# Performance work log

Hardware: AMD Instinct MI355X
Metric: run time of the kernel (lower is better)

## Reference

```python
import jax, jax.numpy as jnp
import numpy as np

N = 50000   # nodes
E = 800000  # edges
H = 128     # hidden_dim
H2 = H // 2


def setup_inputs() -> dict:
    key = jax.random.key(0)
    ks = jax.random.split(key, 12)
    s = 0.05  # weight scale for numerical sanity
    d = {}
    d['coord_x'] = jax.random.normal(ks[0], (N,), jnp.float32)
    d['coord_y'] = jax.random.normal(ks[1], (N,), jnp.float32)
    d['W1'] = jax.random.normal(ks[2], (3, H), jnp.float32) * s
    d['b1'] = jnp.zeros((H,), jnp.float32)
    d['W2'] = jax.random.normal(ks[3], (H, H), jnp.float32) * s
    d['b2'] = jnp.zeros((H,), jnp.float32)
    d['W3'] = jax.random.normal(ks[4], (H, H), jnp.float32) * s
    d['b3'] = jnp.zeros((H,), jnp.float32)
    d['W4'] = jax.random.normal(ks[5], (H, H), jnp.float32) * s
    d['b4'] = jnp.zeros((H,), jnp.float32)
    d['W5'] = jax.random.normal(ks[6], (H, H), jnp.float32) * s
    d['b5'] = jnp.zeros((H,), jnp.float32)
    d['Wl1'] = jax.random.normal(ks[7], (H, H2), jnp.float32) * s
    d['bl1'] = jnp.zeros((H2,), jnp.float32)
    d['Wl2'] = jax.random.normal(ks[8], (H2, 1), jnp.float32) * s
    d['bl2'] = jnp.zeros((1,), jnp.float32)
    d['src'] = jax.random.randint(ks[9], (E,), 0, N, dtype=jnp.int32)
    d['dst'] = jax.random.randint(ks[10], (E,), 0, N, dtype=jnp.int32)
    return d


def reference(coord_x, coord_y, W1, b1, W2, b2, W3, b3, W4, b4, W5, b5,
              Wl1, bl1, Wl2, bl2, src, dst):
    ones_e = jnp.ones((E,), jnp.float32)
    in_deg = jax.ops.segment_sum(ones_e, dst, num_segments=N)   # [N]
    out_deg = jax.ops.segment_sum(ones_e, src, num_segments=N)  # [N]
    # DGL GraphConv norm='both': D_out^{-1/2} on src side, D_in^{-1/2} on dst side,
    # degrees clamped to min 1.
    norm_s = (jnp.maximum(out_deg, 1.0) ** -0.5)[:, None]  # [N,1]
    norm_d = (jnp.maximum(in_deg, 1.0) ** -0.5)[:, None]   # [N,1]

    def gconv(h, W, b):
        msg = (h * norm_s)[src]                                   # [E,F] gather
        agg = jax.ops.segment_sum(msg, dst, num_segments=N)       # [N,F] scatter-add
        return (agg * norm_d) @ W + b

    # node features: [in_degree, x, y]
    h = jnp.stack([in_deg, coord_x, coord_y], axis=1)  # [N,3]
    for W, b in ((W1, b1), (W2, b2), (W3, b3), (W4, b4), (W5, b5)):
        h = jax.nn.relu(gconv(h, W, b))

    graph_emb = jnp.mean(h, axis=0, keepdims=True)          # [1,H] mean_nodes
    h_emb = jax.nn.relu(graph_emb @ Wl1 + bl1)              # dropout p=0 -> identity
    pred = jax.nn.sigmoid(h_emb @ Wl2 + bl2)                # [1,1]
    return pred, graph_emb, h
```

## Files before the change

### kernel.cpp

```cpp
#include <hip/hip_runtime.h>
#include <hip/hip_bf16.h>
#include <math.h>

#define NN 50000
#define NE 800000
#define HD 128
#define NB 196
#define CAP 5120
#define B1_EPB 1024

typedef __attribute__((ext_vector_type(8))) short bf16x8v;
typedef __attribute__((ext_vector_type(4))) float f32x4v;

static __device__ __forceinline__ unsigned short f2bf(float x) {
    union { float f; unsigned u; } v; v.f = x;
    unsigned r = v.u + 0x7fff + ((v.u >> 16) & 1);
    return (unsigned short)(r >> 16);
}

__global__ __launch_bounds__(256) void bucket_kernel(const int* __restrict__ src,
                                                     const int* __restrict__ dst,
                                                     int* __restrict__ dcur,
                                                     int* __restrict__ scur,
                                                     ushort2* __restrict__ dbucket,
                                                     unsigned short* __restrict__ sbucket) {
    __shared__ int hd[NB], hsb[NB], cd[NB], cs[NB];
    int t = threadIdx.x;
    if (t < NB) { hd[t] = 0; hsb[t] = 0; }
    __syncthreads();
    int d[4], s[4];
    int e0 = blockIdx.x * B1_EPB + t;
    #pragma unroll
    for (int j = 0; j < 4; ++j) {
        int e = e0 + j * 256;
        if (e < NE) {
            d[j] = dst[e]; s[j] = src[e];
            atomicAdd(&hd[d[j] >> 8], 1);
            atomicAdd(&hsb[s[j] >> 8], 1);
        } else d[j] = -1;
    }
    __syncthreads();
    if (t < NB) {
        cd[t] = atomicAdd(&dcur[t], hd[t]);
        cs[t] = atomicAdd(&scur[t], hsb[t]);
    }
    __syncthreads();
    #pragma unroll
    for (int j = 0; j < 4; ++j) {
        if (d[j] >= 0) {
            int b = d[j] >> 8;
            int p = atomicAdd(&cd[b], 1);
            if (p < CAP) dbucket[(long)b * CAP + p] = make_ushort2((unsigned short)d[j],
                                                                   (unsigned short)s[j]);
            int bs = s[j] >> 8;
            int p2 = atomicAdd(&cs[bs], 1);
            if (p2 < CAP) sbucket[(long)bs * CAP + p2] = (unsigned short)s[j];
        }
    }
}

__global__ __launch_bounds__(256) void csr_out_kernel(const ushort2* __restrict__ dbucket,
                                                      const int* __restrict__ dcur,
                                                      const unsigned short* __restrict__ sbucket,
                                                      const int* __restrict__ scur,
                                                      int* __restrict__ row_ptr,
                                                      unsigned short* __restrict__ col,
                                                      int* __restrict__ out_cnt) {
    __shared__ int buf[256];
    __shared__ int hist[256];
    __shared__ int cur[256];
    int k = blockIdx.x, t = threadIdx.x;

    int tot = (t < NB) ? min(dcur[t], CAP) : 0;
    buf[t] = tot;
    __syncthreads();
    for (int o = 1; o < 256; o <<= 1) {
        int a = (t >= o) ? buf[t - o] : 0;
        __syncthreads();
        buf[t] += a;
        __syncthreads();
    }
    int base = (k > 0) ? buf[k - 1] : 0;
    int cnt = min(dcur[k], CAP);

    hist[t] = 0;
    __syncthreads();
    const ushort2* bk = dbucket + (long)k * CAP;
    for (int e = t; e < cnt; e += 256) atomicAdd(&hist[bk[e].x & 255], 1);
    __syncthreads();
    int h = hist[t];

    buf[t] = h;
    __syncthreads();
    for (int o = 1; o < 256; o <<= 1) {
        int a = (t >= o) ? buf[t - o] : 0;
        __syncthreads();
        buf[t] += a;
        __syncthreads();
    }
    int start = base + buf[t] - h;
    int id = (k << 8) + t;
    if (id < NN) row_ptr[id] = start;
    if (k == NB - 1 && t == 0) row_ptr[NN] = base + cnt;
    cur[t] = start;
    __syncthreads();

    for (int e = t; e < cnt; e += 256) {
        ushort2 p = bk[e];
        int pos = atomicAdd(&cur[p.x & 255], 1);
        col[pos] = p.y;
    }

    __syncthreads();
    hist[t] = 0;
    __syncthreads();
    int scnt = min(scur[k], CAP);
    const unsigned short* sk = sbucket + (long)k * CAP;
    for (int e = t; e < scnt; e += 256) atomicAdd(&hist[sk[e] & 255], 1);
    __syncthreads();
    if (id < NN) out_cnt[id] = hist[t];
}

__global__ __launch_bounds__(256) void initw_kernel(const float* __restrict__ cx,
                                                    const float* __restrict__ cy,
                                                    const int* __restrict__ row_ptr,
                                                    const int* __restrict__ out_cnt,
                                                    const float* __restrict__ W2,
                                                    const float* __restrict__ W3,
                                                    const float* __restrict__ W4,
                                                    const float* __restrict__ W5,
                                                    float* __restrict__ norm_s,
                                                    float* __restrict__ norm_d,
                                                    float* __restrict__ h0s,
                                                    unsigned short* __restrict__ Wt,
                                                    float* __restrict__ embsum8) {
    int bid = blockIdx.x, t = threadIdx.x;
    if (bid < NB) {
        int i = (bid << 8) + t;
        if (i < NN) {
            float id = (float)(row_ptr[i + 1] - row_ptr[i]);
            float od = (float)out_cnt[i];
            float ns = 1.0f / sqrtf(fmaxf(od, 1.0f));
            norm_s[i] = ns;
            norm_d[i] = 1.0f / sqrtf(fmaxf(id, 1.0f));
            h0s[i * 3 + 0] = id * ns;
            h0s[i * 3 + 1] = cx[i] * ns;
            h0s[i * 3 + 2] = cy[i] * ns;
        }
    } else {
        int gid = ((bid - NB) << 8) + t;
        int l = gid >> 14, idx = gid & 16383;
        int n = idx >> 7, k = idx & 127;
        const float* W = (l == 0) ? W2 : (l == 1) ? W3 : (l == 2) ? W4 : W5;
        Wt[gid] = f2bf(W[k * 128 + n]);
        if (gid < 1024) embsum8[gid] = 0.0f;
    }
}

__global__ __launch_bounds__(256) void layer1_kernel(const int* __restrict__ row_ptr,
                                                     const unsigned short* __restrict__ col,
                                                     const float* __restrict__ h0s,
                                                     const float* __restrict__ norm_d,
                                                     const float* __restrict__ norm_s,
                                                     const float* __restrict__ W1,
                                                     const float* __restrict__ b1,
                                                     unsigned short* __restrict__ h1s) {
    __shared__ float la3[256][3];
    __shared__ float lw[3][128];
    __shared__ float lb[128];
    int t = threadIdx.x;
    int n0 = blockIdx.x << 8;
    if (t < 128) {
        lw[0][t] = W1[t]; lw[1][t] = W1[128 + t]; lw[2][t] = W1[256 + t];
        lb[t] = b1[t];
    }
    int n = n0 + t;
    if (n < NN) {
        float a0 = 0.f, a1 = 0.f, a2 = 0.f;
        int end = row_ptr[n + 1];
        for (int e = row_ptr[n]; e < end; ++e) {
            int s = col[e];
            a0 += h0s[s * 3 + 0];
            a1 += h0s[s * 3 + 1];
            a2 += h0s[s * 3 + 2];
        }
        float nd = norm_d[n];
        la3[t][0] = a0 * nd; la3[t][1] = a1 * nd; la3[t][2] = a2 * nd;
    }
    __syncthreads();
    #pragma unroll 4
    for (int i = 0; i < 128; ++i) {
        int idx = (i << 8) + t;
        int r = idx >> 7, c = idx & 127;
        int nn = n0 + r;
        if (nn < NN) {
            float v = la3[r][0] * lw[0][c] + la3[r][1] * lw[1][c]
                    + la3[r][2] * lw[2][c] + lb[c];
            h1s[((long)nn << 7) + c] = f2bf(fmaxf(v, 0.f) * norm_s[nn]);
        }
    }
}

__global__ __launch_bounds__(256) void fused_layer16_kernel(const int* __restrict__ row_ptr,
                                                            const unsigned short* __restrict__ col,
                                                            const unsigned int* __restrict__ hin,
                                                            const float* __restrict__ norm_d,
                                                            const float* __restrict__ norm_s,
                                                            const unsigned short* __restrict__ Wt,
                                                            const float* __restrict__ bias,
                                                            unsigned short* __restrict__ hout) {
    __shared__ unsigned int lA[16][68];
    int t = threadIdx.x;
    int wv = t >> 6, lane = t & 63;
    int m0 = blockIdx.x << 4;

    const unsigned int* hb = hin + lane;
    int e[4], en[4];
    float ax[4], ay[4];
    #pragma unroll
    for (int i = 0; i < 4; ++i) {
        int n = m0 + (i << 2) + wv;
        e[i] = row_ptr[n]; en[i] = row_ptr[n + 1];
        ax[i] = 0.f; ay[i] = 0.f;
    }

    while (e[0] + 3 < en[0] && e[1] + 3 < en[1] &&
           e[2] + 3 < en[2] && e[3] + 3 < en[3]) {
        unsigned u[16];
        #pragma unroll
        for (int i = 0; i < 4; ++i)
            #pragma unroll
            for (int j = 0; j < 4; ++j)
                u[(i << 2) + j] = hb[(long)col[e[i] + j] << 6];
        #pragma unroll
        for (int i = 0; i < 4; ++i) {
            #pragma unroll
            for (int j = 0; j < 4; ++j) {
                ax[i] += __uint_as_float(u[(i << 2) + j] << 16);
                ay[i] += __uint_as_float(u[(i << 2) + j] & 0xffff0000u);
            }
            e[i] += 4;
        }
    }
    #pragma unroll
    for (int i = 0; i < 4; ++i) {
        for (; e[i] + 3 < en[i]; e[i] += 4) {
            unsigned u[4];
            #pragma unroll
            for (int j = 0; j < 4; ++j) u[j] = hb[(long)col[e[i] + j] << 6];
            #pragma unroll
            for (int j = 0; j < 4; ++j) {
                ax[i] += __uint_as_float(u[j] << 16);
                ay[i] += __uint_as_float(u[j] & 0xffff0000u);
            }
        }
        for (; e[i] < en[i]; ++e[i]) {
            unsigned u0 = hb[(long)col[e[i]] << 6];
            ax[i] += __uint_as_float(u0 << 16);
            ay[i] += __uint_as_float(u0 & 0xffff0000u);
        }
    }
    #pragma unroll
    for (int i = 0; i < 4; ++i) {
        int r = (i << 2) + wv;
        float nd = norm_d[m0 + r];
        lA[r][lane] = (unsigned)f2bf(ax[i] * nd) | ((unsigned)f2bf(ay[i] * nd) << 16);
    }
    __syncthreads();

    int fr = lane & 15, kq = lane >> 4;
    bf16x8v a0 = *(const bf16x8v*)&lA[fr][ 0 + (kq << 2)];
    bf16x8v a1 = *(const bf16x8v*)&lA[fr][16 + (kq << 2)];
    bf16x8v a2 = *(const bf16x8v*)&lA[fr][32 + (kq << 2)];
    bf16x8v a3 = *(const bf16x8v*)&lA[fr][48 + (kq << 2)];

    float4 scv = *(const float4*)(norm_s + m0 + (kq << 2));

    #pragma unroll
    for (int j = 0; j < 2; ++j) {
        int n0 = ((wv << 1) + j) << 4;
        const unsigned short* wb = Wt + ((n0 + fr) << 7) + (kq << 3);
        f32x4v acc = {0.f, 0.f, 0.f, 0.f};
        acc = __builtin_amdgcn_mfma_f32_16x16x32_bf16(a0, *(const bf16x8v*)(wb + 0),  acc, 0, 0, 0);
        acc = __builtin_amdgcn_mfma_f32_16x16x32_bf16(a1, *(const bf16x8v*)(wb + 32), acc, 0, 0, 0);
        acc = __builtin_amdgcn_mfma_f32_16x16x32_bf16(a2, *(const bf16x8v*)(wb + 64), acc, 0, 0, 0);
        acc = __builtin_amdgcn_mfma_f32_16x16x32_bf16(a3, *(const bf16x8v*)(wb + 96), acc, 0, 0, 0);

        int c = n0 + fr;
        float bv = bias[c];
        #pragma unroll
        for (int r = 0; r < 4; ++r) {
            int mr = m0 + (kq << 2) + r;
            float v = fmaxf(acc[r] + bv, 0.f);
            float sc = (r == 0) ? scv.x : (r == 1) ? scv.y : (r == 2) ? scv.z : scv.w;
            hout[((long)mr << 7) + c] = f2bf(v * sc);
        }
    }
}

__global__ __launch_bounds__(256) void gather_bf16_kernel(const int* __restrict__ row_ptr,
                                                          const unsigned short* __restrict__ col,
                                                          const unsigned int* __restrict__ hs2,
                                                          const float* __restrict__ norm_d,
                                                          unsigned int* __restrict__ aggb2) {
    int t = threadIdx.x;
    int wv = t >> 6;
    int lane = t & 63;
    int nA = blockIdx.x * 8 + wv;
    int nB = nA + 4;
    int eA = row_ptr[nA], endA = row_ptr[nA + 1];
    int eB = row_ptr[nB], endB = row_ptr[nB + 1];
    const unsigned int* hb = hs2 + lane;
    float axA = 0.f, ayA = 0.f, axB = 0.f, ayB = 0.f;

    while (eA + 7 < endA && eB + 7 < endB) {
        unsigned uA[8], uB[8];
        #pragma unroll
        for (int j = 0; j < 8; ++j) uA[j] = hb[(long)col[eA + j] << 6];
        #pragma unroll
        for (int j = 0; j < 8; ++j) uB[j] = hb[(long)col[eB + j] << 6];
        #pragma unroll
        for (int j = 0; j < 8; ++j) {
            axA += __uint_as_float(uA[j] << 16);
            ayA += __uint_as_float(uA[j] & 0xffff0000u);
            axB += __uint_as_float(uB[j] << 16);
            ayB += __uint_as_float(uB[j] & 0xffff0000u);
        }
        eA += 8; eB += 8;
    }
    for (; eA + 7 < endA; eA += 8) {
        unsigned u[8];
        #pragma unroll
        for (int j = 0; j < 8; ++j) u[j] = hb[(long)col[eA + j] << 6];
        #pragma unroll
        for (int j = 0; j < 8; ++j) {
            axA += __uint_as_float(u[j] << 16);
            ayA += __uint_as_float(u[j] & 0xffff0000u);
        }
    }
    for (; eA < endA; ++eA) {
        unsigned u0 = hb[(long)col[eA] << 6];
        axA += __uint_as_float(u0 << 16);
        ayA += __uint_as_float(u0 & 0xffff0000u);
    }
    for (; eB + 7 < endB; eB += 8) {
        unsigned u[8];
        #pragma unroll
        for (int j = 0; j < 8; ++j) u[j] = hb[(long)col[eB + j] << 6];
        #pragma unroll
        for (int j = 0; j < 8; ++j) {
            axB += __uint_as_float(u[j] << 16);
            ayB += __uint_as_float(u[j] & 0xffff0000u);
        }
    }
    for (; eB < endB; ++eB) {
        unsigned u0 = hb[(long)col[eB] << 6];
        axB += __uint_as_float(u0 << 16);
        ayB += __uint_as_float(u0 & 0xffff0000u);
    }

    float ndA = norm_d[nA], ndB = norm_d[nB];
    aggb2[(nA << 6) + lane] = (unsigned)f2bf(axA * ndA) | ((unsigned)f2bf(ayA * ndA) << 16);
    aggb2[(nB << 6) + lane] = (unsigned)f2bf(axB * ndB) | ((unsigned)f2bf(ayB * ndB) << 16);
}

__global__ __launch_bounds__(256) void gemm_mfma_kernel(const unsigned short* __restrict__ aggb,
                                                        const unsigned short* __restrict__ Wt,
                                                        const float* __restrict__ bias,
                                                        float* __restrict__ out_f32,
                                                        float* __restrict__ embsum8) {
    __shared__ unsigned short ldsw[128][136];
    __shared__ float ldscol[4][4][128];

    int t = threadIdx.x;
    int wv = t >> 6, lane = t & 63;
    int fr = lane & 15, kq = lane >> 4;
    int m0 = blockIdx.x * 64 + wv * 16;

    #pragma unroll
    for (int i = 0; i < 8; ++i) {
        int idx = t + 256 * i;
        int r = idx >> 4;
        int c8 = (idx & 15) << 3;
        *(bf16x8v*)(&ldsw[r][c8]) = *(const bf16x8v*)(Wt + (r << 7) + c8);
    }

    int mrow = m0 + fr;
    long abase = (long)((mrow < NN) ? mrow : 0) << 7;
    bf16x8v a0 = *(const bf16x8v*)(aggb + abase + 0  + kq * 8);
    bf16x8v a1 = *(const bf16x8v*)(aggb + abase + 32 + kq * 8);
    bf16x8v a2 = *(const bf16x8v*)(aggb + abase + 64 + kq * 8);
    bf16x8v a3 = *(const bf16x8v*)(aggb + abase + 96 + kq * 8);

    __syncthreads();

    #pragma unroll
    for (int nt = 0; nt < 8; ++nt) {
        int n0 = nt << 4;
        f32x4v acc = {0.f, 0.f, 0.f, 0.f};
        acc = __builtin_amdgcn_mfma_f32_16x16x32_bf16(a0, *(const bf16x8v*)(&ldsw[n0 + fr][0  + kq * 8]), acc, 0, 0, 0);
        acc = __builtin_amdgcn_mfma_f32_16x16x32_bf16(a1, *(const bf16x8v*)(&ldsw[n0 + fr][32 + kq * 8]), acc, 0, 0, 0);
        acc = __builtin_amdgcn_mfma_f32_16x16x32_bf16(a2, *(const bf16x8v*)(&ldsw[n0 + fr][64 + kq * 8]), acc, 0, 0, 0);
        acc = __builtin_amdgcn_mfma_f32_16x16x32_bf16(a3, *(const bf16x8v*)(&ldsw[n0 + fr][96 + kq * 8]), acc, 0, 0, 0);

        int c = n0 + fr;
        float bv = bias[c];
        float cs = 0.f;
        #pragma unroll
        for (int r = 0; r < 4; ++r) {
            int mr = m0 + kq * 4 + r;
            if (mr < NN) {
                float v = fmaxf(acc[r] + bv, 0.f);
                out_f32[((long)mr << 7) + c] = v;
                cs += v;
            }
        }
        ldscol[wv][kq][c] = cs;
    }

    __syncthreads();
    if (t < 128) {
        float s = 0.f;
        #pragma unroll
        for (int w = 0; w < 4; ++w)
            #pragma unroll
            for (int q = 0; q < 4; ++q)
                s += ldscol[w][q][t];
        atomicAdd(&embsum8[((blockIdx.x & 7) << 7) + t], s);
    }
}

__global__ __launch_bounds__(128) void head_kernel(const float* __restrict__ embsum8,
                                                   const float* __restrict__ Wl1,
                                                   const float* __restrict__ bl1,
                                                   const float* __restrict__ Wl2,
                                                   const float* __restrict__ bl2,
                                                   float* __restrict__ d_out) {
    __shared__ float emb[128];
    __shared__ float hemb[64];
    int t = threadIdx.x;
    float e = 0.f;
    #pragma unroll
    for (int j = 0; j < 8; ++j) e += embsum8[(j << 7) + t];
    e *= (1.0f / (float)NN);
    emb[t] = e;
    d_out[1 + t] = e;
    __syncthreads();
    if (t < 64) {
        float acc = bl1[t];
        for (int k = 0; k < 128; ++k)
            acc += emb[k] * Wl1[k * 64 + t];
        hemb[t] = fmaxf(acc, 0.f);
    }
    __syncthreads();
    if (t == 0) {
        float acc = bl2[0];
        for (int j = 0; j < 64; ++j)
            acc += hemb[j] * Wl2[j];
        d_out[0] = 1.0f / (1.0f + expf(-acc));
    }
}

extern "C" void kernel_launch(void* const* d_in, const int* in_sizes, int n_in,
                              void* d_out, int out_size, void* d_ws, size_t ws_size,
                              hipStream_t stream) {
    const float* cx  = (const float*)d_in[0];
    const float* cy  = (const float*)d_in[1];
    const float* W1  = (const float*)d_in[2];
    const float* b1  = (const float*)d_in[3];
    const float* W2  = (const float*)d_in[4];
    const float* b2  = (const float*)d_in[5];
    const float* W3  = (const float*)d_in[6];
    const float* b3  = (const float*)d_in[7];
    const float* W4  = (const float*)d_in[8];
    const float* b4  = (const float*)d_in[9];
    const float* W5  = (const float*)d_in[10];
    const float* b5  = (const float*)d_in[11];
    const float* Wl1 = (const float*)d_in[12];
    const float* bl1 = (const float*)d_in[13];
    const float* Wl2 = (const float*)d_in[14];
    const float* bl2 = (const float*)d_in[15];
    const int*   src = (const int*)d_in[16];
    const int*   dst = (const int*)d_in[17];

    float* out = (float*)d_out;
    float* h_out = out + 129;

    float* ws       = (float*)d_ws;
    float* norm_s   = ws;
    float* norm_d   = ws + NN;
    int*   out_cnt  = (int*)(ws + 2 * NN);
    int*   row_ptr  = (int*)(ws + 3 * NN);
    unsigned short* hsA = (unsigned short*)(ws + 4 * NN + 64);
    unsigned short* hsB = (unsigned short*)(ws + 68 * NN + 64);
    unsigned short* col = (unsigned short*)(ws + 132 * NN + 64);
    float* h0s      = ws + 148 * NN + 64;
    unsigned short* Wt = (unsigned short*)(ws + 154 * NN + 64);
    float* embsum8  = ws + 154 * NN + 64 + 32768;
    int*   dcur     = (int*)(ws + 154 * NN + 34112);
    int*   scur     = dcur + NB;
    ushort2* dbucket = (ushort2*)(ws + 154 * NN + 34560);
    unsigned short* sbucket = (unsigned short*)(ws + 154 * NN + 34560 + NB * CAP);

    hipMemsetAsync(dcur, 0, 2 * NB * sizeof(int), stream);
    bucket_kernel<<<(NE + B1_EPB - 1) / B1_EPB, 256, 0, stream>>>(src, dst, dcur, scur,
                                                                  dbucket, sbucket);
    csr_out_kernel<<<NB, 256, 0, stream>>>(dbucket, dcur, sbucket, scur,
                                           row_ptr, col, out_cnt);

    initw_kernel<<<NB + 256, 256, 0, stream>>>(cx, cy, row_ptr, out_cnt,
                                               W2, W3, W4, W5,
                                               norm_s, norm_d, h0s, Wt, embsum8);

    layer1_kernel<<<(NN + 255) / 256, 256, 0, stream>>>(row_ptr, col, h0s,
                                                        norm_d, norm_s, W1, b1, hsA);

    const float* bs[3] = {b2, b3, b4};
    unsigned short* hcur = hsA;
    unsigned short* hnxt = hsB;
    for (int l = 0; l < 3; ++l) {
        fused_layer16_kernel<<<NN / 16, 256, 0, stream>>>(
            row_ptr, col, (const unsigned int*)hcur, norm_d, norm_s,
            Wt + l * 16384, bs[l], hnxt);
        unsigned short* tmp = hcur; hcur = hnxt; hnxt = tmp;
    }

    gather_bf16_kernel<<<NN / 8, 256, 0, stream>>>(row_ptr, col,
                                                   (const unsigned int*)hcur,
                                                   norm_d,
                                                   (unsigned int*)hnxt);
    gemm_mfma_kernel<<<(NN + 63) / 64, 256, 0, stream>>>(hnxt, Wt + 3 * 16384, b5,
                                                         h_out, embsum8);

    head_kernel<<<1, 128, 0, stream>>>(embsum8, Wl1, bl1, Wl2, bl2, out);
}
```

Before: 290.8 us.

## Process nodes in degree-sorted order to balance per-block gather work

Builds a degree histogram during CSR construction, scans it, and adds a permsort kernel that writes a permutation of node ids ordered by descending in-degree. The fused layer and gather kernels now look up node ids through this permutation, so rows of similar degree share a block and warps waste fewer idle lanes on uneven neighbor loops. The cost is an extra kernel, extra atomics, and indirect, non-contiguous output writes and norm lookups.

```diff
diff --git a/kernel.cpp b/kernel.cpp
--- a/kernel.cpp
+++ b/kernel.cpp
@@ -65,11 +65,14 @@
                                                       const int* __restrict__ scur,
                                                       int* __restrict__ row_ptr,
                                                       unsigned short* __restrict__ col,
-                                                      int* __restrict__ out_cnt) {
+                                                      int* __restrict__ out_cnt,
+                                                      int* __restrict__ degbins) {
     __shared__ int buf[256];
     __shared__ int hist[256];
     __shared__ int cur[256];
+    __shared__ int dh[64];
     int k = blockIdx.x, t = threadIdx.x;
+    if (t < 64) dh[t] = 0;
 
     int tot = (t < NB) ? min(dcur[t], CAP) : 0;
     buf[t] = tot;
@@ -100,7 +103,10 @@
     }
     int start = base + buf[t] - h;
     int id = (k << 8) + t;
-    if (id < NN) row_ptr[id] = start;
+    if (id < NN) {
+        row_ptr[id] = start;
+        atomicAdd(&dh[63 - min(h, 63)], 1);
+    }
     if (k == NB - 1 && t == 0) row_ptr[NN] = base + cnt;
     cur[t] = start;
     __syncthreads();
@@ -119,6 +125,7 @@
     for (int e = t; e < scnt; e += 256) atomicAdd(&hist[sk[e] & 255], 1);
     __syncthreads();
     if (id < NN) out_cnt[id] = hist[t];
+    if (t < 64 && dh[t]) atomicAdd(&degbins[t], dh[t]);
 }
 
 __global__ __launch_bounds__(256) void initw_kernel(const float* __restrict__ cx,
@@ -133,7 +140,9 @@
                                                     float* __restrict__ norm_d,
                                                     float* __restrict__ h0s,
                                                     unsigned short* __restrict__ Wt,
-                                                    float* __restrict__ embsum8) {
+                                                    float* __restrict__ embsum8,
+                                                    const int* __restrict__ degbins,
+                                                    int* __restrict__ bincur) {
     int bid = blockIdx.x, t = threadIdx.x;
     if (bid < NB) {
         int i = (bid << 8) + t;
@@ -154,6 +163,35 @@
         const float* W = (l == 0) ? W2 : (l == 1) ? W3 : (l == 2) ? W4 : W5;
         Wt[gid] = f2bf(W[k * 128 + n]);
         if (gid < 1024) embsum8[gid] = 0.0f;
+        if (bid == NB && t == 0) {
+            int run = 0;
+            for (int b = 0; b < 64; ++b) { bincur[b] = run; run += degbins[b]; }
+        }
+    }
+}
+
+__global__ __launch_bounds__(256) void permsort_kernel(const int* __restrict__ row_ptr,
+                                                       int* __restrict__ bincur,
+                                                       int* __restrict__ perm) {
+    __shared__ int lh[64], lbase[64];
+    int k = blockIdx.x, t = threadIdx.x;
+    if (t < 64) lh[t] = 0;
+    __syncthreads();
+    int id = (k << 8) + t;
+    int bin = 0;
+    if (id < NN) {
+        int deg = row_ptr[id + 1] - row_ptr[id];
+        bin = 63 - min(deg, 63);
+        atomicAdd(&lh[bin], 1);
+    }
+    __syncthreads();
+    if (t < 64) lbase[t] = lh[t] ? atomicAdd(&bincur[t], lh[t]) : 0;
+    __syncthreads();
+    if (t < 64) lh[t] = 0;
+    __syncthreads();
+    if (id < NN) {
+        int pos = lbase[bin] + atomicAdd(&lh[bin], 1);
+        perm[pos] = id;
     }
 }
 
@@ -206,21 +244,31 @@
                                                             const unsigned int* __restrict__ hin,
                                                             const float* __restrict__ norm_d,
                                                             const float* __restrict__ norm_s,
+                                                            const int* __restrict__ perm,
                                                             const unsigned short* __restrict__ Wt,
                                                             const float* __restrict__ bias,
                                                             unsigned short* __restrict__ hout) {
     __shared__ unsigned int lA[16][68];
+    __shared__ int lPerm[16];
+    __shared__ float lNs[16];
     int t = threadIdx.x;
     int wv = t >> 6, lane = t & 63;
     int m0 = blockIdx.x << 4;
 
+    if (t < 16) {
+        int p = perm[m0 + t];
+        lPerm[t] = p;
+        lNs[t] = norm_s[p];
+    }
+    __syncthreads();
+
     const unsigned int* hb = hin + lane;
-    int e[4], en[4];
+    int e[4], en[4], nid[4];
     float ax[4], ay[4];
     #pragma unroll
     for (int i = 0; i < 4; ++i) {
-        int n = m0 + (i << 2) + wv;
-        e[i] = row_ptr[n]; en[i] = row_ptr[n + 1];
+        nid[i] = lPerm[(i << 2) + wv];
+        e[i] = row_ptr[nid[i]]; en[i] = row_ptr[nid[i] + 1];
         ax[i] = 0.f; ay[i] = 0.f;
     }
 
@@ -263,7 +311,7 @@
     #pragma unroll
     for (int i = 0; i < 4; ++i) {
         int r = (i << 2) + wv;
-        float nd = norm_d[m0 + r];
+        float nd = norm_d[nid[i]];
         lA[r][lane] = (unsigned)f2bf(ax[i] * nd) | ((unsigned)f2bf(ay[i] * nd) << 16);
     }
     __syncthreads();
@@ -273,8 +321,6 @@
     bf16x8v a1 = *(const bf16x8v*)&lA[fr][16 + (kq << 2)];
     bf16x8v a2 = *(const bf16x8v*)&lA[fr][32 + (kq << 2)];
     bf16x8v a3 = *(const bf16x8v*)&lA[fr][48 + (kq << 2)];
-
-    float4 scv = *(const float4*)(norm_s + m0 + (kq << 2));
 
     #pragma unroll
     for (int j = 0; j < 2; ++j) {
@@ -290,10 +336,10 @@
         float bv = bias[c];
         #pragma unroll
         for (int r = 0; r < 4; ++r) {
-            int mr = m0 + (kq << 2) + r;
+            int slot = (kq << 2) + r;
+            int mr = lPerm[slot];
             float v = fmaxf(acc[r] + bv, 0.f);
-            float sc = (r == 0) ? scv.x : (r == 1) ? scv.y : (r == 2) ? scv.z : scv.w;
-            hout[((long)mr << 7) + c] = f2bf(v * sc);
+            hout[((long)mr << 7) + c] = f2bf(v * lNs[slot]);
         }
     }
 }
@@ -302,12 +348,14 @@
                                                           const unsigned short* __restrict__ col,
                                                           const unsigned int* __restrict__ hs2,
                                                           const float* __restrict__ norm_d,
+                                                          const int* __restrict__ perm,
                                                           unsigned int* __restrict__ aggb2) {
     int t = threadIdx.x;
     int wv = t >> 6;
     int lane = t & 63;
-    int nA = blockIdx.x * 8 + wv;
-    int nB = nA + 4;
+    int base = blockIdx.x * 8;
+    int nA = perm[base + wv];
+    int nB = perm[base + wv + 4];
     int eA = row_ptr[nA], endA = row_ptr[nA + 1];
     int eB = row_ptr[nB], endB = row_ptr[nB + 1];
     const unsigned int* hb = hs2 + lane;
@@ -360,8 +408,8 @@
     }
 
     float ndA = norm_d[nA], ndB = norm_d[nB];
-    aggb2[(nA << 6) + lane] = (unsigned)f2bf(axA * ndA) | ((unsigned)f2bf(ayA * ndA) << 16);
-    aggb2[(nB << 6) + lane] = (unsigned)f2bf(axB * ndB) | ((unsigned)f2bf(ayB * ndB) << 16);
+    aggb2[((long)nA << 6) + lane] = (unsigned)f2bf(axA * ndA) | ((unsigned)f2bf(ayA * ndA) << 16);
+    aggb2[((long)nB << 6) + lane] = (unsigned)f2bf(axB * ndB) | ((unsigned)f2bf(ayB * ndB) << 16);
 }
 
 __global__ __launch_bounds__(256) void gemm_mfma_kernel(const unsigned short* __restrict__ aggb,
@@ -495,23 +543,28 @@
     unsigned short* hsB = (unsigned short*)(ws + 68 * NN + 64);
     unsigned short* col = (unsigned short*)(ws + 132 * NN + 64);
     float* h0s      = ws + 148 * NN + 64;
+    int*   perm     = (int*)(ws + 151 * NN + 64);
     unsigned short* Wt = (unsigned short*)(ws + 154 * NN + 64);
     float* embsum8  = ws + 154 * NN + 64 + 32768;
     int*   dcur     = (int*)(ws + 154 * NN + 34112);
     int*   scur     = dcur + NB;
-    ushort2* dbucket = (ushort2*)(ws + 154 * NN + 34560);
-    unsigned short* sbucket = (unsigned short*)(ws + 154 * NN + 34560 + NB * CAP);
-
-    hipMemsetAsync(dcur, 0, 2 * NB * sizeof(int), stream);
+    int*   degbins  = dcur + 2 * NB;
+    int*   bincur   = degbins + 64;
+    ushort2* dbucket = (ushort2*)(ws + 154 * NN + 34760);
+    unsigned short* sbucket = (unsigned short*)(ws + 154 * NN + 34760 + NB * CAP);
+
+    hipMemsetAsync(dcur, 0, (2 * NB + 128) * sizeof(int), stream);
     bucket_kernel<<<(NE + B1_EPB - 1) / B1_EPB, 256, 0, stream>>>(src, dst, dcur, scur,
                                                                   dbucket, sbucket);
     csr_out_kernel<<<NB, 256, 0, stream>>>(dbucket, dcur, sbucket, scur,
-                                           row_ptr, col, out_cnt);
+                                           row_ptr, col, out_cnt, degbins);
 
     initw_kernel<<<NB + 256, 256, 0, stream>>>(cx, cy, row_ptr, out_cnt,
                                                W2, W3, W4, W5,
-                                               norm_s, norm_d, h0s, Wt, embsum8);
-
+                                               norm_s, norm_d, h0s, Wt, embsum8,
+                                               degbins, bincur);
+
+    permsort_kernel<<<NB, 256, 0, stream>>>(row_ptr, bincur, perm);
     layer1_kernel<<<(NN + 255) / 256, 256, 0, stream>>>(row_ptr, col, h0s,
                                                         norm_d, norm_s, W1, b1, hsA);
 
@@ -520,14 +573,14 @@
     unsigned short* hnxt = hsB;
     for (int l = 0; l < 3; ++l) {
         fused_layer16_kernel<<<NN / 16, 256, 0, stream>>>(
-            row_ptr, col, (const unsigned int*)hcur, norm_d, norm_s,
+            row_ptr, col, (const unsigned int*)hcur, norm_d, norm_s, perm,
             Wt + l * 16384, bs[l], hnxt);
         unsigned short* tmp = hcur; hcur = hnxt; hnxt = tmp;
     }
 
     gather_bf16_kernel<<<NN / 8, 256, 0, stream>>>(row_ptr, col,
                                                    (const unsigned int*)hcur,
-                                                   norm_d,
+                                                   norm_d, perm,
                                                    (unsigned int*)hnxt);
     gemm_mfma_kernel<<<(NN + 63) / 64, 256, 0, stream>>>(hnxt, Wt + 3 * 16384, b5,
                                                          h_out, embsum8);
```

After: 292.9 us. Within noise of the previous version (+0.7%).
